# Kernel tuning notes

Measured on AMD Instinct MI355X. Metric: run time of the kernel, lower is better.

## Reference

```python
import jax, jax.numpy as jnp
import numpy as np

EMBED = 768
HIDDEN = 768
HEADS = 12
HEAD_DIM = HIDDEN // HEADS


def setup_inputs() -> dict:
    key = jax.random.key(0)
    ks = jax.random.split(key, 9)
    B, S = 16, 512
    lim = 1.0 / np.sqrt(EMBED)
    def lin(kw, kb):
        W = jax.random.uniform(kw, (EMBED, HIDDEN), jnp.float32, -lim, lim)
        b = jax.random.uniform(kb, (HIDDEN,), jnp.float32, -lim, lim)
        return W, b
    Wq, bq = lin(ks[0], ks[1])
    Wk, bk = lin(ks[2], ks[3])
    Wv, bv = lin(ks[4], ks[5])
    inp = jax.random.normal(ks[6], (B, S, EMBED), jnp.float32)
    mask = jax.random.randint(ks[7], (B, S), 0, 2).astype(jnp.float32)
    return {"input": inp, "input_mask": mask,
            "Wq": Wq, "bq": bq, "Wk": Wk, "bk": bk, "Wv": Wv, "bv": bv}


def reference(input, input_mask, Wq, bq, Wk, bk, Wv, bv):
    B, S, _ = input.shape
    # projections -> (B, H, S, D)
    def proj(W, b):
        x = jnp.einsum('bse,eh->bsh', input, W) + b
        return x.reshape(B, S, HEADS, HEAD_DIM).transpose(0, 2, 1, 3)
    Q = proj(Wq, bq)
    K = proj(Wk, bk)
    V = proj(Wv, bv)
    # scores (B, H, S, S), additive mask over keys
    scores = jnp.einsum('bhqd,bhkd->bhqk', Q, K) / jnp.sqrt(jnp.float32(HEAD_DIM))
    bias = (input_mask * -1e9)[:, None, None, :]  # (B,1,1,S) broadcast over heads & queries
    weight = jax.nn.softmax(scores + bias, axis=-1)
    out = jnp.einsum('bhqk,bhkd->bhqd', weight, V)
    return out.transpose(0, 2, 1, 3).reshape(B, S, HIDDEN)
```

## Files before the change

### kernel.cpp

```cpp
#include <hip/hip_runtime.h>
#include <hip/hip_bf16.h>
#include <cstdint>
#include <cstddef>

#define B_  16
#define S_  512
#define E_  768
#define NH_ 12
#define D_  64
#define M_  (B_*S_)

typedef unsigned short u16;
typedef __attribute__((ext_vector_type(4))) float f32x4;
typedef __attribute__((ext_vector_type(8))) short bf16x8;

#define LOG2E 1.4426950408889634f

__device__ __forceinline__ u16 f2bf(float f){
  union { float fv; uint32_t u; } v; v.fv = f;
  uint32_t u = v.u;
  uint32_t r = u + 0x7fffu + ((u >> 16) & 1u);
  return (u16)(r >> 16);
}

__global__ __launch_bounds__(256) void prep_kernel(
    const float* __restrict__ X, u16* __restrict__ Xb,
    const float* __restrict__ Wq, const float* __restrict__ Wk,
    const float* __restrict__ Wv, u16* __restrict__ WtBase)
{
  __shared__ float t[32][33];
  const int bx = blockIdx.x;
  if (bx < 6144){
    int i = bx * 256 + threadIdx.x;
    float4 v = reinterpret_cast<const float4*>(X)[i];
    ushort4 o;
    o.x = f2bf(v.x); o.y = f2bf(v.y); o.z = f2bf(v.z); o.w = f2bf(v.w);
    reinterpret_cast<ushort4*>(Xb)[i] = o;
  } else {
    int tt = bx - 6144;
    int z = tt / 576, rem = tt % 576;
    int byi = rem / 24, bxi = rem % 24;
    const float* W = (z == 0) ? Wq : ((z == 1) ? Wk : Wv);
    u16* Wt = WtBase + (size_t)z * E_ * E_;
    int bx0 = bxi * 32, by0 = byi * 32;
    int tx = threadIdx.x & 31, ty = threadIdx.x >> 5;
    #pragma unroll
    for (int i = 0; i < 32; i += 8)
      t[ty + i][tx] = W[(size_t)(by0 + ty + i) * E_ + bx0 + tx];
    __syncthreads();
    #pragma unroll
    for (int i = 0; i < 32; i += 8)
      Wt[(size_t)(bx0 + ty + i) * E_ + by0 + tx] = f2bf(t[tx][ty + i]);
  }
}

__global__ __launch_bounds__(256) void qkv_gemm_kernel(
    const u16* __restrict__ Xb, const u16* __restrict__ WtBase,
    const float* __restrict__ bq, const float* __restrict__ bk, const float* __restrict__ bv,
    u16* __restrict__ Qb, u16* __restrict__ Kb, u16* __restrict__ VtB)
{
  __shared__ u16 lA[16 * 512];
  __shared__ u16 lB[16 * 512];
  const int z = blockIdx.z;
  const u16* Wt = WtBase + (size_t)z * E_ * E_;
  const float* bias = (z == 0) ? bq : ((z == 1) ? bk : bv);
  const int m0 = blockIdx.x * 128;
  const int n0 = blockIdx.y * 128;
  const int tid = threadIdx.x;
  const int lane = tid & 63;
  const int wave = tid >> 6;
  const int wm = wave & 1, wn = wave >> 1;
  const int col0 = lane & 15, quad = lane >> 4;
  const int srow = lane >> 2, soct = lane & 3;
  const int sslot = soct*16 + (srow ^ (soct << 1));
  const int rslot = quad*16 + (col0 ^ (quad << 1));

  f32x4 acc[4][4];
  #pragma unroll
  for (int i = 0; i < 4; ++i)
    #pragma unroll
    for (int j = 0; j < 4; ++j)
      acc[i][j] = (f32x4){0.f, 0.f, 0.f, 0.f};

  #pragma unroll 1
  for (int k0 = 0; k0 < E_; k0 += 64){
    __syncthreads();
    uint4 va[4], vb[4];
    #pragma unroll
    for (int i = 0; i < 4; ++i){
      int rh = i >> 1, kh = i & 1;
      int grow = rh*64 + wave*16 + srow;
      va[i] = *reinterpret_cast<const uint4*>(Xb + (size_t)(m0 + grow) * E_ + k0 + kh*32 + soct*8);
      vb[i] = *reinterpret_cast<const uint4*>(Wt + (size_t)(n0 + grow) * E_ + k0 + kh*32 + soct*8);
    }
    #pragma unroll
    for (int i = 0; i < 4; ++i){
      int rh = i >> 1, kh = i & 1;
      int c = (rh*4 + wave)*2 + kh;
      *reinterpret_cast<uint4*>(&lA[c*512 + sslot*8]) = va[i];
      *reinterpret_cast<uint4*>(&lB[c*512 + sslot*8]) = vb[i];
    }
    __syncthreads();
    #pragma unroll
    for (int ks = 0; ks < 2; ++ks){
      bf16x8 af[4], bfr[4];
      #pragma unroll
      for (int mi = 0; mi < 4; ++mi)
        af[mi] = *reinterpret_cast<const bf16x8*>(&lA[((wm*4 + mi)*2 + ks)*512 + rslot*8]);
      #pragma unroll
      for (int ni = 0; ni < 4; ++ni)
        bfr[ni] = *reinterpret_cast<const bf16x8*>(&lB[((wn*4 + ni)*2 + ks)*512 + rslot*8]);
      #pragma unroll
      for (int mi = 0; mi < 4; ++mi)
        #pragma unroll
        for (int ni = 0; ni < 4; ++ni)
          acc[mi][ni] = __builtin_amdgcn_mfma_f32_16x16x32_bf16(af[mi], bfr[ni], acc[mi][ni], 0, 0, 0);
    }
  }

  #pragma unroll
  for (int mi = 0; mi < 4; ++mi){
    #pragma unroll
    for (int ni = 0; ni < 4; ++ni){
      int n = n0 + wn*64 + ni*16 + col0;
      float bval = bias[n];
      int h = n >> 6, d = n & 63;
      #pragma unroll
      for (int r = 0; r < 4; ++r){
        int m = m0 + wm*64 + mi*16 + quad*4 + r;
        int b = m >> 9, s = m & 511;
        u16 obf = f2bf(acc[mi][ni][r] + bval);
        size_t bh = (size_t)b * NH_ + h;
        if (z == 0)      Qb[(bh * S_ + s) * D_ + d] = obf;
        else if (z == 1) Kb[(bh * S_ + s) * D_ + d] = obf;
        else             VtB[(bh * D_ + d) * S_ + s] = obf;
      }
    }
  }
}

__global__ __launch_bounds__(256) void attn_kernel(
    const u16* __restrict__ Qb, const u16* __restrict__ Kb, const u16* __restrict__ VtB,
    const float* __restrict__ mask, float* __restrict__ out)
{
  __shared__ u16 lK[2][8 * 512];
  __shared__ u16 lV[2][8 * 512];
  __shared__ u16 lP[8 * 1024];
  __shared__ float biasS[S_];
  const int bh = blockIdx.x;
  const int qt = blockIdx.y;
  const int b = bh / NH_, h = bh % NH_;
  const int tid = threadIdx.x, lane = tid & 63, wave = tid >> 6;
  const int col0 = lane & 15, quad = lane >> 4;
  const int ls = lane & 15, lk = lane >> 4;
  const float C1 = 0.125f * LOG2E;

  for (int i = tid; i < S_; i += 256)
    biasS[i] = mask[b * S_ + i] * (-1.0e9f * LOG2E);

  const u16* Kbh = Kb  + (size_t)bh * S_ * D_;
  const u16* Vbh = VtB + (size_t)bh * D_ * S_;

  bf16x8 qf[2][2];
  #pragma unroll
  for (int g = 0; g < 2; ++g){
    int qrow = qt*128 + wave*32 + g*16 + col0;
    #pragma unroll
    for (int ks = 0; ks < 2; ++ks)
      qf[g][ks] = *reinterpret_cast<const bf16x8*>(
          Qb + ((size_t)bh * S_ + qrow) * D_ + ks*32 + quad*8);
  }

  uint4 rg[4];
  auto issue = [&](int st){
    if (wave < 2){
      #pragma unroll
      for (int gg = 0; gg < 4; ++gg){
        int c = wave*4 + gg, ks = c >> 2, nt = c & 3;
        rg[gg] = *reinterpret_cast<const uint4*>(
            Kbh + (size_t)(st*64 + nt*16 + ls) * D_ + ks*32 + lk*8);
      }
    } else {
      #pragma unroll
      for (int gg = 0; gg < 4; ++gg){
        int c = (wave - 2)*4 + gg, ks2 = c >> 2, nd = c & 3;
        rg[gg] = *reinterpret_cast<const uint4*>(
            Vbh + (size_t)(nd*16 + ls) * S_ + st*64 + ks2*32 + lk*8);
      }
    }
  };
  issue(0);

  f32x4 o[2][4];
  #pragma unroll
  for (int g = 0; g < 2; ++g)
    #pragma unroll
    for (int i = 0; i < 4; ++i) o[g][i] = (f32x4){0.f, 0.f, 0.f, 0.f};
  float psum[2] = {0.f, 0.f};

  #pragma unroll 1
  for (int st = 0; st < 8; ++st){
    const int cur = st & 1;
    if (wave < 2){
      #pragma unroll
      for (int gg = 0; gg < 4; ++gg)
        *reinterpret_cast<uint4*>(&lK[cur][(wave*4 + gg)*512 + lane*8]) = rg[gg];
    } else {
      #pragma unroll
      for (int gg = 0; gg < 4; ++gg)
        *reinterpret_cast<uint4*>(&lV[cur][((wave - 2)*4 + gg)*512 + lane*8]) = rg[gg];
    }
    __syncthreads();
    if (st < 7) issue(st + 1);

    f32x4 sc[2][4];
    #pragma unroll
    for (int g = 0; g < 2; ++g)
      #pragma unroll
      for (int nt = 0; nt < 4; ++nt) sc[g][nt] = (f32x4){0.f, 0.f, 0.f, 0.f};
    #pragma unroll
    for (int ks = 0; ks < 2; ++ks){
      bf16x8 kf[4];
      #pragma unroll
      for (int nt = 0; nt < 4; ++nt)
        kf[nt] = *reinterpret_cast<const bf16x8*>(&lK[cur][(ks*4 + nt)*512 + lane*8]);
      #pragma unroll
      for (int g = 0; g < 2; ++g)
        #pragma unroll
        for (int nt = 0; nt < 4; ++nt)
          sc[g][nt] = __builtin_amdgcn_mfma_f32_16x16x32_bf16(kf[nt], qf[g][ks], sc[g][nt], 0, 0, 0);
    }

    float4 bb[4];
    #pragma unroll
    for (int nt = 0; nt < 4; ++nt)
      bb[nt] = *reinterpret_cast<const float4*>(&biasS[st*64 + nt*16 + quad*4]);

    #pragma unroll
    for (int g = 0; g < 2; ++g){
      #pragma unroll
      for (int nt = 0; nt < 4; ++nt){
        float p0 = exp2f(sc[g][nt][0] * C1 + bb[nt].x);
        float p1 = exp2f(sc[g][nt][1] * C1 + bb[nt].y);
        float p2 = exp2f(sc[g][nt][2] * C1 + bb[nt].z);
        float p3 = exp2f(sc[g][nt][3] * C1 + bb[nt].w);
        psum[g] += (p0 + p1) + (p2 + p3);
        float2 ab; ab.x = p0; ab.y = p1;
        float2 cd; cd.x = p2; cd.y = p3;
        __hip_bfloat162 h01 = __float22bfloat162_rn(ab);
        __hip_bfloat162 h23 = __float22bfloat162_rn(cd);
        uint2 pw;
        pw.x = *reinterpret_cast<unsigned int*>(&h01);
        pw.y = *reinterpret_cast<unsigned int*>(&h23);
        int addr = (wave*2 + g)*1024 + (nt >> 1)*512
                 + (((nt & 1)*2 + (quad >> 1))*16 + col0)*8 + (quad & 1)*4;
        *reinterpret_cast<uint2*>(&lP[addr]) = pw;
      }
    }

    #pragma unroll
    for (int ks2 = 0; ks2 < 2; ++ks2){
      bf16x8 pf0 = *reinterpret_cast<const bf16x8*>(&lP[(wave*2 + 0)*1024 + ks2*512 + lane*8]);
      bf16x8 pf1 = *reinterpret_cast<const bf16x8*>(&lP[(wave*2 + 1)*1024 + ks2*512 + lane*8]);
      #pragma unroll
      for (int nd = 0; nd < 4; ++nd){
        bf16x8 vf = *reinterpret_cast<const bf16x8*>(&lV[cur][(ks2*4 + nd)*512 + lane*8]);
        o[0][nd] = __builtin_amdgcn_mfma_f32_16x16x32_bf16(pf0, vf, o[0][nd], 0, 0, 0);
        o[1][nd] = __builtin_amdgcn_mfma_f32_16x16x32_bf16(pf1, vf, o[1][nd], 0, 0, 0);
      }
    }
  }

  #pragma unroll
  for (int g = 0; g < 2; ++g){
    float tot = psum[g];
    tot += __shfl_xor(tot, 16, 64);
    tot += __shfl_xor(tot, 32, 64);
    #pragma unroll
    for (int r = 0; r < 4; ++r){
      int s = qt*128 + wave*32 + g*16 + quad*4 + r;
      float lr = __shfl(tot, (lane & 48) | (quad*4 + r), 64);
      float inv = 1.0f / lr;
      #pragma unroll
      for (int nd = 0; nd < 4; ++nd){
        int d = nd*16 + col0;
        out[((size_t)b * S_ + s) * E_ + h*D_ + d] = o[g][nd][r] * inv;
      }
    }
  }
}

extern "C" void kernel_launch(void* const* d_in, const int* in_sizes, int n_in,
                              void* d_out, int out_size, void* d_ws, size_t ws_size,
                              hipStream_t stream){
  const float* X    = (const float*)d_in[0];
  const float* mask = (const float*)d_in[1];
  const float* Wq   = (const float*)d_in[2];
  const float* bq   = (const float*)d_in[3];
  const float* Wk   = (const float*)d_in[4];
  const float* bk   = (const float*)d_in[5];
  const float* Wv   = (const float*)d_in[6];
  const float* bv   = (const float*)d_in[7];
  float* out = (float*)d_out;

  u16* Xb = (u16*)d_ws;
  u16* Wt = Xb + (size_t)M_ * E_;
  u16* Qb = Wt + (size_t)3 * E_ * E_;
  u16* Kb = Qb + (size_t)M_ * E_;
  u16* Vt = Kb + (size_t)M_ * E_;

  prep_kernel<<<6144 + 1728, 256, 0, stream>>>(X, Xb, Wq, Wk, Wv, Wt);
  qkv_gemm_kernel<<<dim3(64, 6, 3), 256, 0, stream>>>(Xb, Wt, bq, bk, bv, Qb, Kb, Vt);
  attn_kernel<<<dim3(192, 4), 256, 0, stream>>>(Qb, Kb, Vt, mask, out);
}
```

Measured before the change: 197.1 us.

## Double-buffer QKV GEMM LDS with register prefetch and coalesce attention K/V loads

The QKV projection GEMM now uses a 32-wide K step with two LDS buffers. The next tile's global loads are issued into registers before the current tile's MFMAs, so there is one barrier per iteration instead of two. The attention kernel's K/V tile loads switch to a row-major lane mapping (4 lanes per 64-byte row) with the same XOR-swizzled LDS slots the GEMM uses, which gives more coalesced global reads and fewer bank conflicts. The trade-off is more loop iterations, each with less MFMA work, and a slightly different LDS addressing scheme.

```diff
diff --git a/kernel.cpp b/kernel.cpp
--- a/kernel.cpp
+++ b/kernel.cpp
@@ -59,8 +59,8 @@
     const float* __restrict__ bq, const float* __restrict__ bk, const float* __restrict__ bv,
     u16* __restrict__ Qb, u16* __restrict__ Kb, u16* __restrict__ VtB)
 {
-  __shared__ u16 lA[16 * 512];
-  __shared__ u16 lB[16 * 512];
+  __shared__ u16 lA[2][8 * 512];
+  __shared__ u16 lB[2][8 * 512];
   const int z = blockIdx.z;
   const u16* Wt = WtBase + (size_t)z * E_ * E_;
   const float* bias = (z == 0) ? bq : ((z == 1) ? bk : bv);
@@ -82,40 +82,40 @@
     for (int j = 0; j < 4; ++j)
       acc[i][j] = (f32x4){0.f, 0.f, 0.f, 0.f};
 
+  uint4 va[2], vb[2];
+  auto issue = [&](int k0){
+    #pragma unroll
+    for (int cc = 0; cc < 2; ++cc){
+      int c = wave * 2 + cc;
+      va[cc] = *reinterpret_cast<const uint4*>(Xb + (size_t)(m0 + c*16 + srow) * E_ + k0 + soct*8);
+      vb[cc] = *reinterpret_cast<const uint4*>(Wt + (size_t)(n0 + c*16 + srow) * E_ + k0 + soct*8);
+    }
+  };
+  issue(0);
+
   #pragma unroll 1
-  for (int k0 = 0; k0 < E_; k0 += 64){
+  for (int it = 0; it < 24; ++it){
+    const int cur = it & 1;
+    #pragma unroll
+    for (int cc = 0; cc < 2; ++cc){
+      int c = wave * 2 + cc;
+      *reinterpret_cast<uint4*>(&lA[cur][c*512 + sslot*8]) = va[cc];
+      *reinterpret_cast<uint4*>(&lB[cur][c*512 + sslot*8]) = vb[cc];
+    }
     __syncthreads();
-    uint4 va[4], vb[4];
-    #pragma unroll
-    for (int i = 0; i < 4; ++i){
-      int rh = i >> 1, kh = i & 1;
-      int grow = rh*64 + wave*16 + srow;
-      va[i] = *reinterpret_cast<const uint4*>(Xb + (size_t)(m0 + grow) * E_ + k0 + kh*32 + soct*8);
-      vb[i] = *reinterpret_cast<const uint4*>(Wt + (size_t)(n0 + grow) * E_ + k0 + kh*32 + soct*8);
-    }
-    #pragma unroll
-    for (int i = 0; i < 4; ++i){
-      int rh = i >> 1, kh = i & 1;
-      int c = (rh*4 + wave)*2 + kh;
-      *reinterpret_cast<uint4*>(&lA[c*512 + sslot*8]) = va[i];
-      *reinterpret_cast<uint4*>(&lB[c*512 + sslot*8]) = vb[i];
-    }
-    __syncthreads();
-    #pragma unroll
-    for (int ks = 0; ks < 2; ++ks){
-      bf16x8 af[4], bfr[4];
-      #pragma unroll
-      for (int mi = 0; mi < 4; ++mi)
-        af[mi] = *reinterpret_cast<const bf16x8*>(&lA[((wm*4 + mi)*2 + ks)*512 + rslot*8]);
+    if (it + 1 < 24) issue((it + 1) * 32);
+    bf16x8 af[4], bfr[4];
+    #pragma unroll
+    for (int mi = 0; mi < 4; ++mi)
+      af[mi] = *reinterpret_cast<const bf16x8*>(&lA[cur][(wm*4 + mi)*512 + rslot*8]);
+    #pragma unroll
+    for (int ni = 0; ni < 4; ++ni)
+      bfr[ni] = *reinterpret_cast<const bf16x8*>(&lB[cur][(wn*4 + ni)*512 + rslot*8]);
+    #pragma unroll
+    for (int mi = 0; mi < 4; ++mi)
       #pragma unroll
       for (int ni = 0; ni < 4; ++ni)
-        bfr[ni] = *reinterpret_cast<const bf16x8*>(&lB[((wn*4 + ni)*2 + ks)*512 + rslot*8]);
-      #pragma unroll
-      for (int mi = 0; mi < 4; ++mi)
-        #pragma unroll
-        for (int ni = 0; ni < 4; ++ni)
-          acc[mi][ni] = __builtin_amdgcn_mfma_f32_16x16x32_bf16(af[mi], bfr[ni], acc[mi][ni], 0, 0, 0);
-    }
+        acc[mi][ni] = __builtin_amdgcn_mfma_f32_16x16x32_bf16(af[mi], bfr[ni], acc[mi][ni], 0, 0, 0);
   }
 
   #pragma unroll
@@ -152,7 +152,9 @@
   const int b = bh / NH_, h = bh % NH_;
   const int tid = threadIdx.x, lane = tid & 63, wave = tid >> 6;
   const int col0 = lane & 15, quad = lane >> 4;
-  const int ls = lane & 15, lk = lane >> 4;
+  const int srow = lane >> 2, soct = lane & 3;
+  const int sslot = soct*16 + (srow ^ (soct << 1));
+  const int rslot = quad*16 + (col0 ^ (quad << 1));
   const float C1 = 0.125f * LOG2E;
 
   for (int i = tid; i < S_; i += 256)
@@ -178,14 +180,14 @@
       for (int gg = 0; gg < 4; ++gg){
         int c = wave*4 + gg, ks = c >> 2, nt = c & 3;
         rg[gg] = *reinterpret_cast<const uint4*>(
-            Kbh + (size_t)(st*64 + nt*16 + ls) * D_ + ks*32 + lk*8);
+            Kbh + (size_t)(st*64 + nt*16 + srow) * D_ + ks*32 + soct*8);
       }
     } else {
       #pragma unroll
       for (int gg = 0; gg < 4; ++gg){
         int c = (wave - 2)*4 + gg, ks2 = c >> 2, nd = c & 3;
         rg[gg] = *reinterpret_cast<const uint4*>(
-            Vbh + (size_t)(nd*16 + ls) * S_ + st*64 + ks2*32 + lk*8);
+            Vbh + (size_t)(nd*16 + srow) * S_ + st*64 + ks2*32 + soct*8);
       }
     }
   };
@@ -204,11 +206,11 @@
     if (wave < 2){
       #pragma unroll
       for (int gg = 0; gg < 4; ++gg)
-        *reinterpret_cast<uint4*>(&lK[cur][(wave*4 + gg)*512 + lane*8]) = rg[gg];
+        *reinterpret_cast<uint4*>(&lK[cur][(wave*4 + gg)*512 + sslot*8]) = rg[gg];
     } else {
       #pragma unroll
       for (int gg = 0; gg < 4; ++gg)
-        *reinterpret_cast<uint4*>(&lV[cur][((wave - 2)*4 + gg)*512 + lane*8]) = rg[gg];
+        *reinterpret_cast<uint4*>(&lV[cur][((wave - 2)*4 + gg)*512 + sslot*8]) = rg[gg];
     }
     __syncthreads();
     if (st < 7) issue(st + 1);
@@ -223,7 +225,7 @@
       bf16x8 kf[4];
       #pragma unroll
       for (int nt = 0; nt < 4; ++nt)
-        kf[nt] = *reinterpret_cast<const bf16x8*>(&lK[cur][(ks*4 + nt)*512 + lane*8]);
+        kf[nt] = *reinterpret_cast<const bf16x8*>(&lK[cur][(ks*4 + nt)*512 + rslot*8]);
       #pragma unroll
       for (int g = 0; g < 2; ++g)
         #pragma unroll
@@ -264,7 +266,7 @@
       bf16x8 pf1 = *reinterpret_cast<const bf16x8*>(&lP[(wave*2 + 1)*1024 + ks2*512 + lane*8]);
       #pragma unroll
       for (int nd = 0; nd < 4; ++nd){
-        bf16x8 vf = *reinterpret_cast<const bf16x8*>(&lV[cur][(ks2*4 + nd)*512 + lane*8]);
+        bf16x8 vf = *reinterpret_cast<const bf16x8*>(&lV[cur][(ks2*4 + nd)*512 + rslot*8]);
         o[0][nd] = __builtin_amdgcn_mfma_f32_16x16x32_bf16(pf0, vf, o[0][nd], 0, 0, 0);
         o[1][nd] = __builtin_amdgcn_mfma_f32_16x16x32_bf16(pf1, vf, o[1][nd], 0, 0, 0);
       }
```

New measurement: 284.5 us. 44.3% more time.
